# Kernel optimization log

Measured on AMD Instinct MI355X. Metric: run time of the kernel, lower is better.

Reference implementation:

```python
import jax, jax.numpy as jnp
import numpy as np

N_NODES = 50000
N_EDGES = 800000
F_DIM = 35   # num_features = in_channels = out_channels
K_HOPS = 3   # num_filters (diffusion order)


def _dconv(xcat, src, dst, w_fwd, w_bwd, theta, bias, n):
    """Dual-direction diffusion convolution: sum_k T_fwd^k X theta[0,k] + T_bwd^k X theta[1,k] + b.
    xcat: [n, Cin]; theta: [2, K, Cin, Cout]; w_fwd/w_bwd: [E] normalized edge weights."""
    out = xcat @ (theta[0, 0] + theta[1, 0]) + bias  # k=0 term (identity hop)
    xf = xcat
    xb = xcat
    for k in range(1, theta.shape[1]):
        # forward diffusion: aggregate src -> dst with out-degree normalization
        xf = jax.ops.segment_sum(w_fwd[:, None] * xf[src], dst, num_segments=n)
        # backward diffusion: aggregate dst -> src with in-degree normalization
        xb = jax.ops.segment_sum(w_bwd[:, None] * xb[dst], src, num_segments=n)
        out = out + xf @ theta[0, k] + xb @ theta[1, k]
    return out


def _cell(x, h, src, dst, wf, wb, tz, bz, tr, br, tc, bc, n):
    """DCRNN GRU cell with diffusion convolutions as the gate transforms."""
    xh = jnp.concatenate([x, h], axis=-1)  # [n, 2F]
    z = jax.nn.sigmoid(_dconv(xh, src, dst, wf, wb, tz, bz, n))
    r = jax.nn.sigmoid(_dconv(xh, src, dst, wf, wb, tr, br, n))
    c = jnp.tanh(_dconv(jnp.concatenate([x, r * h], axis=-1), src, dst, wf, wb, tc, bc, n))
    return z * h + (1.0 - z) * c


def setup_inputs() -> dict:
    key = jax.random.key(0)
    ks = jax.random.split(key, 12)
    x = jax.random.normal(ks[0], (N_NODES, F_DIM), dtype=jnp.float32)
    edge_index = jax.random.randint(ks[1], (2, N_EDGES), 0, N_NODES)
    edge_weight = jax.random.uniform(ks[2], (N_EDGES,), dtype=jnp.float32)
    cin = 2 * F_DIM
    s = 1.0 / np.sqrt(cin)
    u = lambda k, sh: jax.random.uniform(k, sh, jnp.float32, -s, s)
    theta_z = u(ks[3], (2, K_HOPS, cin, F_DIM)); b_z = u(ks[4], (F_DIM,))
    theta_r = u(ks[5], (2, K_HOPS, cin, F_DIM)); b_r = u(ks[6], (F_DIM,))
    theta_c = u(ks[7], (2, K_HOPS, cin, F_DIM)); b_c = u(ks[8], (F_DIM,))
    sl = 1.0 / np.sqrt(F_DIM)
    W_lin = jax.random.uniform(ks[9], (F_DIM, 1), jnp.float32, -sl, sl)
    b_lin = jax.random.uniform(ks[10], (1,), jnp.float32, -sl, sl)
    return dict(x=x, edge_index=edge_index, edge_weight=edge_weight,
                theta_z=theta_z, b_z=b_z, theta_r=theta_r, b_r=b_r,
                theta_c=theta_c, b_c=b_c, W_lin=W_lin, b_lin=b_lin)


def reference(x, edge_index, edge_weight, theta_z, b_z, theta_r, b_r, theta_c, b_c, W_lin, b_lin):
    n = x.shape[0]
    src, dst = edge_index[0], edge_index[1]
    # learned/normalized adjacency A (forward + backward transition weights)
    deg_out = jax.ops.segment_sum(edge_weight, src, num_segments=n)
    deg_in = jax.ops.segment_sum(edge_weight, dst, num_segments=n)
    wf = edge_weight / jnp.where(deg_out[src] > 0, deg_out[src], 1.0)
    wb = edge_weight / jnp.where(deg_in[dst] > 0, deg_in[dst], 1.0)
    A = jnp.stack([wf, wb])  # [2, E]
    h = jnp.zeros_like(x)
    # recurrent cell called twice (second call reuses hidden state and A)
    h = _cell(x, h, src, dst, wf, wb, theta_z, b_z, theta_r, b_r, theta_c, b_c, n)
    h = _cell(x, h, src, dst, wf, wb, theta_z, b_z, theta_r, b_r, theta_c, b_c, n)
    out = jax.nn.relu(h @ W_lin + b_lin)  # [n, 1]
    return out, A
```

## Files before the change

### kernel.cpp

```cpp
#include <hip/hip_runtime.h>
#include <hip/hip_fp16.h>

#define NF 35
#define HS 36
#define TMAT 2450
#define ZCOLS 384
#define ZUSED 360
#define CCOLS 192
#define CUSED 180


__global__ void degree2_k(const int* __restrict__ src, const int* __restrict__ dst,
                          unsigned int* __restrict__ cntF2, unsigned int* __restrict__ cntB2,
                          int* __restrict__ rankF, int* __restrict__ rankB, int E) {
    int e = blockIdx.x * blockDim.x + threadIdx.x;
    if (e < E) {
        int d = dst[e], s = src[e];
        int shd = (d & 1) * 16, shs = (s & 1) * 16;
        unsigned int o1 = atomicAdd(&cntF2[d >> 1], 1u << shd);
        rankF[e] = (int)((o1 >> shd) & 0xFFFFu);
        unsigned int o2 = atomicAdd(&cntB2[s >> 1], 1u << shs);
        rankB[e] = (int)((o2 >> shs) & 0xFFFFu);
    }
}

__global__ __launch_bounds__(1024) void scan2_k(const unsigned int* __restrict__ cntF2,
                                                const unsigned int* __restrict__ cntB2,
                                                int* __restrict__ rowF,
                                                int* __restrict__ rowB, int n) {
    const unsigned int* cnt = blockIdx.x ? cntB2 : cntF2;
    int* row = blockIdx.x ? rowB : rowF;
    __shared__ int wsum[16];
    __shared__ int carry_s;
    int lane = threadIdx.x & 63, wid = threadIdx.x >> 6;
    if (threadIdx.x == 0) carry_s = 0;
    __syncthreads();
    for (int base = 0; base < n; base += 1024) {
        int i = base + threadIdx.x;
        int v = 0;
        if (i < n) v = (int)((cnt[i >> 1] >> ((i & 1) * 16)) & 0xFFFFu);
        int s = v;
        for (int off = 1; off < 64; off <<= 1) {
            int t = __shfl_up(s, off, 64);
            if (lane >= off) s += t;
        }
        if (lane == 63) wsum[wid] = s;
        __syncthreads();
        if (wid == 0) {
            int t = (lane < 16) ? wsum[lane] : 0;
            int ss = t;
            for (int off = 1; off < 16; off <<= 1) {
                int u = __shfl_up(ss, off, 64);
                if (lane >= off) ss += u;
            }
            if (lane < 16) wsum[lane] = ss - t;
        }
        __syncthreads();
        if (i < n) row[i] = carry_s + wsum[wid] + s - v;
        __syncthreads();
        if (threadIdx.x == 1023) carry_s += wsum[15] + s;
        __syncthreads();
    }
    if (threadIdx.x == 0) row[n] = carry_s;
}

__global__ void scatter2_k(const int* __restrict__ src, const int* __restrict__ dst,
                           const float* __restrict__ w,
                           const int* __restrict__ rankF, const int* __restrict__ rankB,
                           const int* __restrict__ rowF, const int* __restrict__ rowB,
                           int2* __restrict__ pairF, int2* __restrict__ pairB, int E) {
    int e = blockIdx.x * blockDim.x + threadIdx.x;
    if (e < E) {
        int s = src[e], d = dst[e];
        int wb = __float_as_int(w[e]);
        pairF[rowF[d] + rankF[e]] = make_int2(s, wb);
        pairB[rowB[s] + rankB[e]] = make_int2(d, wb);
    }
}

__global__ void segdeg_k(const int* __restrict__ rowF, const int* __restrict__ rowB,
                         const int2* __restrict__ pairF, const int2* __restrict__ pairB,
                         float* __restrict__ deg_in, float* __restrict__ deg_out, int n) {
    int i = blockIdx.x * blockDim.x + threadIdx.x;
    if (i >= n) return;
    float a = 0.f;
    for (int p = rowF[i]; p < rowF[i + 1]; ++p) a += __int_as_float(pairF[p].y);
    deg_in[i] = a;
    float b = 0.f;
    for (int p = rowB[i]; p < rowB[i + 1]; ++p) b += __int_as_float(pairB[p].y);
    deg_out[i] = b;
}

__global__ void norm_k(const int* __restrict__ src, const int* __restrict__ dst,
                       const float* __restrict__ w, const float* __restrict__ deg_out,
                       const float* __restrict__ deg_in,
                       const int2* __restrict__ pairF, const int2* __restrict__ pairB,
                       unsigned int* __restrict__ pFp, unsigned int* __restrict__ pBp,
                       float* __restrict__ wf, float* __restrict__ wb, int E) {
    int e = blockIdx.x * blockDim.x + threadIdx.x;
    if (e >= E) return;
    float ww = w[e];
    float a = deg_out[src[e]];
    float b = deg_in[dst[e]];
    wf[e] = ww / (a > 0.f ? a : 1.f);
    wb[e] = ww / (b > 0.f ? b : 1.f);
    int2 pa = pairF[e];
    float da = deg_out[pa.x];
    float wa = __int_as_float(pa.y) / (da > 0.f ? da : 1.f);
    pFp[e] = (unsigned int)pa.x |
             ((unsigned int)__half_as_ushort(__float2half_rn(wa)) << 16);
    int2 pb = pairB[e];
    float db = deg_in[pb.x];
    float wbv = __int_as_float(pb.y) / (db > 0.f ? db : 1.f);
    pBp[e] = (unsigned int)pb.x |
             ((unsigned int)__half_as_ushort(__float2half_rn(wbv)) << 16);
}


__global__ void pack_k(const float* __restrict__ tz, const float* __restrict__ tr_,
                       const float* __restrict__ tc, const float* __restrict__ bz,
                       const float* __restrict__ br, const float* __restrict__ bc,
                       float* __restrict__ PZ, float* __restrict__ PC) {
    int i = blockIdx.x * 256 + threadIdx.x;
    const int tot1 = 71 * ZCOLS;
    if (i < tot1) {
        int r = i / ZCOLS, j = i - r * ZCOLS;
        int s = j / 36, jl = j - s * 36;
        float v = 0.f;
        if (s < 10 && jl < 35) {
            int zr = s & 1;
            const float* th = zr ? tr_ : tz;
            int grp = s >> 1;
            if (r < 70) {
                if (grp == 0) v = th[r * 35 + jl] + th[3 * TMAT + r * 35 + jl];
                else {
                    int off = (grp == 1) ? 1 : (grp == 2) ? 2 : (grp == 3) ? 4 : 5;
                    v = th[off * TMAT + r * 35 + jl];
                }
            } else if (grp == 0) {
                v = zr ? br[jl] : bz[jl];
            }
        }
        PZ[i] = v;
    } else {
        int i2 = i - tot1;
        if (i2 < 71 * CCOLS) {
            int r = i2 / CCOLS, j = i2 - r * CCOLS;
            int s = j / 36, jl = j - s * 36;
            float v = 0.f;
            if (s < 5 && jl < 35) {
                if (r < 70) {
                    if (s == 0) v = tc[r * 35 + jl] + tc[3 * TMAT + r * 35 + jl];
                    else {
                        int off = (s == 1) ? 1 : (s == 2) ? 2 : (s == 3) ? 4 : 5;
                        v = tc[off * TMAT + r * 35 + jl];
                    }
                } else if (s == 0) v = bc[jl];
            }
            PC[i2] = v;
        }
    }
}


__device__ __forceinline__ uint2 pack4h(float4 a) {
    __half2 lo = __floats2half2_rn(a.x, a.y);
    __half2 hi = __floats2half2_rn(a.z, a.w);
    uint2 r;
    r.x = *(unsigned int*)&lo;
    r.y = *(unsigned int*)&hi;
    return r;
}

__device__ __forceinline__ void fma2h(float* a, unsigned int v, float w) {
    float2 f = __half22float2(*(__half2*)&v);
    a[0] += w * f.x;
    a[1] += w * f.y;
}

__device__ __forceinline__ void fma4u2(float* a, uint2 v, float w) {
    fma2h(a, v.x, w);
    fma2h(a + 2, v.y, w);
}

__device__ __forceinline__ void ld4h(float* a, const char* p) {
    uint2 v = *(const uint2*)p;
    a[0] = 0.f; a[1] = 0.f; a[2] = 0.f; a[3] = 0.f;
    fma4u2(a, v, 1.f);
}

__device__ __forceinline__ void st4h(const float* a, char* p) {
    *(uint2*)p = pack4h(make_float4(a[0], a[1], a[2], a[3]));
}

__device__ __forceinline__ float hw(unsigned int e) {
    return __half2float(__ushort_as_half((unsigned short)(e >> 16)));
}

__device__ __forceinline__ void gath8(float* acc, const char* slab, int off,
                                      const int* __restrict__ rp,
                                      const unsigned int* __restrict__ pp, int row) {
    int p = rp[row], p1 = rp[row + 1];
    for (; p + 3 < p1; p += 4) {
        unsigned int e0 = pp[p], e1 = pp[p + 1], e2 = pp[p + 2], e3 = pp[p + 3];
        uint2 v0 = *(const uint2*)(slab + (size_t)(e0 & 0xFFFFu) * 72 + off);
        uint2 v1 = *(const uint2*)(slab + (size_t)(e1 & 0xFFFFu) * 72 + off);
        uint2 v2 = *(const uint2*)(slab + (size_t)(e2 & 0xFFFFu) * 72 + off);
        uint2 v3 = *(const uint2*)(slab + (size_t)(e3 & 0xFFFFu) * 72 + off);
        fma4u2(acc, v0, hw(e0));
        fma4u2(acc, v1, hw(e1));
        fma4u2(acc, v2, hw(e2));
        fma4u2(acc, v3, hw(e3));
    }
    for (; p < p1; ++p) {
        unsigned int e0 = pp[p];
        uint2 v0 = *(const uint2*)(slab + (size_t)(e0 & 0xFFFFu) * 72 + off);
        fma4u2(acc, v0, hw(e0));
    }
}


template <int WCOLS, int USED>
__device__ __forceinline__ void gemm_store(const float* sxr, const float* __restrict__ W,
                                           char* OUT, size_t slb, int grow, bool valid,
                                           int wid, int kdim) {
#pragma unroll
    for (int jt = 0; jt < WCOLS / 64; ++jt) {
        int j0 = __builtin_amdgcn_readfirstlane(jt * 64 + wid * 16);
        if (j0 >= USED) continue;
        const float4* bw = (const float4*)(W + (size_t)70 * WCOLS + j0);
        float4 a0 = bw[0], a1 = bw[1], a2 = bw[2], a3 = bw[3];
        for (int c = 0; c < kdim; ++c) {
            float v = sxr[c];
            const float4* wr = (const float4*)(W + (size_t)c * WCOLS + j0);
            float4 w0 = wr[0], w1 = wr[1], w2 = wr[2], w3 = wr[3];
            a0.x += v * w0.x; a0.y += v * w0.y; a0.z += v * w0.z; a0.w += v * w0.w;
            a1.x += v * w1.x; a1.y += v * w1.y; a1.z += v * w1.z; a1.w += v * w1.w;
            a2.x += v * w2.x; a2.y += v * w2.y; a2.z += v * w2.z; a2.w += v * w2.w;
            a3.x += v * w3.x; a3.y += v * w3.y; a3.z += v * w3.z; a3.w += v * w3.w;
        }
        if (valid) {
            float4 as[4] = {a0, a1, a2, a3};
#pragma unroll
            for (int g = 0; g < 4; ++g) {
                int jc = j0 + 4 * g;
                if (jc >= USED) break;
                int s = jc / 36, off = jc - s * 36;
                *(uint2*)(OUT + (size_t)s * slb + (size_t)grow * 72 + off * 2) =
                    pack4h(as[g]);
            }
        }
    }
}


template <int H0>
__global__ __launch_bounds__(256) void mm_z_k(const float* __restrict__ x,
                                              const float* __restrict__ h,
                                              const float* __restrict__ W,
                                              char* __restrict__ zS, int n) {
    __shared__ float sx[64 * 73];
    int row0 = blockIdx.x * 64;
    for (int t = threadIdx.x; t < 64 * 35; t += 256) {
        int rl = t / 35, c = t - rl * 35;
        int grow = row0 + rl;
        sx[rl * 73 + c] = (grow < n) ? x[(size_t)grow * 35 + c] : 0.f;
    }
    if (!H0) {
        for (int t = threadIdx.x; t < 64 * 35; t += 256) {
            int rl = t / 35, c = t - rl * 35;
            int grow = row0 + rl;
            sx[rl * 73 + 35 + c] = (grow < n) ? h[(size_t)grow * HS + c] : 0.f;
        }
    }
    __syncthreads();
    int lane = threadIdx.x & 63;
    int wid = threadIdx.x >> 6;
    int grow = row0 + lane;
    gemm_store<ZCOLS, ZUSED>(&sx[lane * 73], W, zS, (size_t)n * 72, grow, grow < n,
                             wid, H0 ? 35 : 70);
}


__global__ __launch_bounds__(256) void mmc_k(const float* __restrict__ x,
                                             const float* __restrict__ h,
                                             const char* __restrict__ zS,
                                             const float* __restrict__ W,
                                             char* __restrict__ cS, int n) {
    __shared__ float sx[64 * 73];
    size_t slb = (size_t)n * 72;
    int row0 = blockIdx.x * 64;
    for (int t = threadIdx.x; t < 64 * 35; t += 256) {
        int rl = t / 35, c = t - rl * 35;
        int grow = row0 + rl;
        sx[rl * 73 + c] = (grow < n) ? x[(size_t)grow * 35 + c] : 0.f;
    }
    for (int t = threadIdx.x; t < 64 * 35; t += 256) {
        int rl = t / 35, c = t - rl * 35;
        int grow = row0 + rl;
        float v = 0.f;
        if (grow < n) {
            float r = __half2float(*(const __half*)(zS + slb + (size_t)grow * 72 + 2 * c));
            v = r * h[(size_t)grow * HS + c];
        }
        sx[rl * 73 + 35 + c] = v;
    }
    __syncthreads();
    int lane = threadIdx.x & 63;
    int wid = threadIdx.x >> 6;
    int grow = row0 + lane;
    gemm_store<CCOLS, CUSED>(&sx[lane * 73], W, cS, slb, grow, grow < n, wid, 70);
}


__global__ __launch_bounds__(256) void hopAz_k(char* __restrict__ zS,
                                               const int* __restrict__ rowF,
                                               const int* __restrict__ rowB,
                                               const unsigned int* __restrict__ pF,
                                               const unsigned int* __restrict__ pB,
                                               int n) {
    int i = blockIdx.x * 256 + threadIdx.x;
    if (i >= n * 9) return;
    size_t slb = (size_t)n * 72;
    int pass = blockIdx.y;
    const int* rp = (pass < 2) ? rowF : rowB;
    const unsigned int* pp = (pass < 2) ? pF : pB;
    int dstS = (pass == 0) ? 2 : (pass == 1) ? 3 : (pass == 2) ? 6 : 7;
    int srcS = dstS + 2;
    int row = i / 9, t = i - row * 9;
    int off = 8 * t;
    char* wp = zS + (size_t)dstS * slb + (size_t)row * 72 + off;
    float acc[4];
    ld4h(acc, wp);
    gath8(acc, zS + (size_t)srcS * slb, off, rp, pp, row);
    st4h(acc, wp);
}

__global__ __launch_bounds__(256) void hopBz_k(char* __restrict__ zS,
                                               const int* __restrict__ rowF,
                                               const int* __restrict__ rowB,
                                               const unsigned int* __restrict__ pF,
                                               const unsigned int* __restrict__ pB,
                                               int n) {
    int i = blockIdx.x * 256 + threadIdx.x;
    if (i >= n * 9) return;
    size_t slb = (size_t)n * 72;
    int g = blockIdx.y;
    int row = i / 9, t = i - row * 9;
    int off = 8 * t;
    char* wp = zS + (size_t)g * slb + (size_t)row * 72 + off;
    float acc[4];
    ld4h(acc, wp);
    gath8(acc, zS + (size_t)(2 + g) * slb, off, rowF, pF, row);
    gath8(acc, zS + (size_t)(6 + g) * slb, off, rowB, pB, row);
#pragma unroll
    for (int k = 0; k < 4; ++k) acc[k] = 1.f / (1.f + expf(-acc[k]));
    st4h(acc, wp);
}

__global__ __launch_bounds__(256) void hopAc_k(char* __restrict__ cS,
                                               const int* __restrict__ rowF,
                                               const int* __restrict__ rowB,
                                               const unsigned int* __restrict__ pF,
                                               const unsigned int* __restrict__ pB,
                                               int n) {
    int i = blockIdx.x * 256 + threadIdx.x;
    if (i >= n * 9) return;
    size_t slb = (size_t)n * 72;
    int pass = blockIdx.y;
    const int* rp = pass ? rowB : rowF;
    const unsigned int* pp = pass ? pB : pF;
    int dstS = pass ? 3 : 1;
    int srcS = pass ? 4 : 2;
    int row = i / 9, t = i - row * 9;
    int off = 8 * t;
    char* wp = cS + (size_t)dstS * slb + (size_t)row * 72 + off;
    float acc[4];
    ld4h(acc, wp);
    gath8(acc, cS + (size_t)srcS * slb, off, rp, pp, row);
    st4h(acc, wp);
}

__global__ __launch_bounds__(256) void hopBcg_k(const char* __restrict__ cS,
                                                const char* __restrict__ zS,
                                                const int* __restrict__ rowF,
                                                const int* __restrict__ rowB,
                                                const unsigned int* __restrict__ pF,
                                                const unsigned int* __restrict__ pB,
                                                float* __restrict__ h, int n) {
    int i = blockIdx.x * 256 + threadIdx.x;
    if (i >= n * 9) return;
    size_t slb = (size_t)n * 72;
    int row = i / 9, t = i - row * 9;
    int off = 8 * t;
    float acc[4];
    ld4h(acc, cS + (size_t)row * 72 + off);
    gath8(acc, cS + slb, off, rowF, pF, row);
    gath8(acc, cS + 3 * slb, off, rowB, pB, row);
    float zv[4];
    ld4h(zv, zS + (size_t)row * 72 + off);
    float* hp = h + (size_t)row * HS + 4 * t;
    float4 h4 = *(float4*)hp;
    float hv[4] = {h4.x, h4.y, h4.z, h4.w};
#pragma unroll
    for (int k = 0; k < 4; ++k) {
        float c = tanhf(acc[k]);
        hv[k] = zv[k] * hv[k] + (1.f - zv[k]) * c;
    }
    *(float4*)hp = make_float4(hv[0], hv[1], hv[2], hv[3]);
}


__global__ void final_k(const float* __restrict__ h, const float* __restrict__ Wl,
                        const float* __restrict__ bl, float* __restrict__ out, int n) {
    int i = blockIdx.x * blockDim.x + threadIdx.x;
    if (i < n) {
        float s = bl[0];
        const float* hr = h + (size_t)i * HS;
#pragma unroll
        for (int j = 0; j < NF; j++) s += hr[j] * Wl[j];
        out[i] = fmaxf(s, 0.f);
    }
}


extern "C" void kernel_launch(void* const* d_in, const int* in_sizes, int n_in,
                              void* d_out, int out_size, void* d_ws, size_t ws_size,
                              hipStream_t stream) {
    const float* x   = (const float*)d_in[0];
    const int*   ei  = (const int*)d_in[1];
    const float* w   = (const float*)d_in[2];
    const float* tz  = (const float*)d_in[3];
    const float* bz  = (const float*)d_in[4];
    const float* tr_ = (const float*)d_in[5];
    const float* br  = (const float*)d_in[6];
    const float* tc  = (const float*)d_in[7];
    const float* bc  = (const float*)d_in[8];
    const float* Wl  = (const float*)d_in[9];
    const float* bl  = (const float*)d_in[10];

    const int n = in_sizes[0] / NF;
    const int E = in_sizes[2];
    const int* src = ei;
    const int* dst = ei + E;

    float* out = (float*)d_out;
    float* wf = out + n;
    float* wb = wf + E;

    char* p = (char*)d_ws;
    auto alloc = [&](size_t bytes) {
        char* r = p;
        p += (bytes + 15) & ~(size_t)15;
        return r;
    };
    int2* pairF = (int2*)alloc((size_t)E * 8);
    int2* pairB = (int2*)alloc((size_t)E * 8);
    unsigned int* pFp = (unsigned int*)alloc((size_t)E * 4);
    unsigned int* pBp = (unsigned int*)alloc((size_t)E * 4);
    int* rowF = (int*)alloc((size_t)(n + 1) * 4);
    int* rowB = (int*)alloc((size_t)(n + 1) * 4);
    unsigned int* cntF2 = (unsigned int*)alloc((size_t)((n + 1) / 2 + 4) * 4);
    unsigned int* cntB2 = (unsigned int*)alloc((size_t)((n + 1) / 2 + 4) * 4);
    float* deg_in  = (float*)alloc((size_t)n * 4);
    float* deg_out = (float*)alloc((size_t)n * 4);
    float* h  = (float*)alloc((size_t)n * HS * 4);
    char* zS  = alloc((size_t)n * 72 * 10);
    char* cS  = alloc((size_t)n * 72 * 5);
    float* PZ = (float*)alloc((size_t)71 * ZCOLS * 4);
    float* PC = (float*)alloc((size_t)71 * CCOLS * 4);
    int* rankF = (int*)zS;
    int* rankB = rankF + E;

    const int gridE = (E + 255) / 256;
    const int gridN = (n + 255) / 256;
    const int g64 = (n + 63) / 64;
    const int g9 = (n * 9 + 255) / 256;
    const size_t cntBytes = ((size_t)((n + 1) / 2 + 4) * 4 + 15) & ~(size_t)15;

    hipMemsetAsync(cntF2, 0, 2 * cntBytes, stream);
    hipMemsetAsync(h, 0, (size_t)n * HS * sizeof(float), stream);
    degree2_k<<<gridE, 256, 0, stream>>>(src, dst, cntF2, cntB2, rankF, rankB, E);
    scan2_k<<<2, 1024, 0, stream>>>(cntF2, cntB2, rowF, rowB, n);
    scatter2_k<<<gridE, 256, 0, stream>>>(src, dst, w, rankF, rankB, rowF, rowB,
                                          pairF, pairB, E);
    segdeg_k<<<gridN, 256, 0, stream>>>(rowF, rowB, pairF, pairB, deg_in, deg_out, n);
    norm_k<<<gridE, 256, 0, stream>>>(src, dst, w, deg_out, deg_in, pairF, pairB,
                                      pFp, pBp, wf, wb, E);
    pack_k<<<(71 * (ZCOLS + CCOLS) + 255) / 256, 256, 0, stream>>>(tz, tr_, tc,
                                                                   bz, br, bc, PZ, PC);

    mm_z_k<1><<<g64, 256, 0, stream>>>(x, h, PZ, zS, n);
    hopAz_k<<<dim3(g9, 4), 256, 0, stream>>>(zS, rowF, rowB, pFp, pBp, n);
    hopBz_k<<<dim3(g9, 2), 256, 0, stream>>>(zS, rowF, rowB, pFp, pBp, n);
    mmc_k<<<g64, 256, 0, stream>>>(x, h, zS, PC, cS, n);
    hopAc_k<<<dim3(g9, 2), 256, 0, stream>>>(cS, rowF, rowB, pFp, pBp, n);
    hopBcg_k<<<g9, 256, 0, stream>>>(cS, zS, rowF, rowB, pFp, pBp, h, n);
    mm_z_k<0><<<g64, 256, 0, stream>>>(x, h, PZ, zS, n);
    hopAz_k<<<dim3(g9, 4), 256, 0, stream>>>(zS, rowF, rowB, pFp, pBp, n);
    hopBz_k<<<dim3(g9, 2), 256, 0, stream>>>(zS, rowF, rowB, pFp, pBp, n);
    mmc_k<<<g64, 256, 0, stream>>>(x, h, zS, PC, cS, n);
    hopAc_k<<<dim3(g9, 2), 256, 0, stream>>>(cS, rowF, rowB, pFp, pBp, n);
    hopBcg_k<<<g9, 256, 0, stream>>>(cS, zS, rowF, rowB, pFp, pBp, h, n);

    final_k<<<gridN, 256, 0, stream>>>(h, Wl, bl, out, n);
}
```

Baseline: 676.2 us.

## Split GEMM column tiles across grid and pair z/r gathers per edge

The GEMM kernels now assign one 64-column tile per block via a second grid dimension instead of looping over all column tiles in each block, raising parallelism. The z and r hop gathers are merged so each edge index and weight is read once and used for two slabs, halving index traffic. The c-gate hop A kernel now does both directions in one thread instead of two grid passes. Each sx tile is now reloaded into shared memory once per column block, and the per-thread gather loads grow.

```diff
diff --git a/kernel.cpp b/kernel.cpp
--- a/kernel.cpp
+++ b/kernel.cpp
@@ -219,36 +219,61 @@
     }
 }
 
+__device__ __forceinline__ void gath8x2(float* a1, float* a2, const char* s1b,
+                                        const char* s2b, int off,
+                                        const int* __restrict__ rp,
+                                        const unsigned int* __restrict__ pp, int row) {
+    int p = rp[row], p1 = rp[row + 1];
+    for (; p + 3 < p1; p += 4) {
+        unsigned int e0 = pp[p], e1 = pp[p + 1], e2 = pp[p + 2], e3 = pp[p + 3];
+        size_t b0 = (size_t)(e0 & 0xFFFFu) * 72 + off;
+        size_t b1 = (size_t)(e1 & 0xFFFFu) * 72 + off;
+        size_t b2 = (size_t)(e2 & 0xFFFFu) * 72 + off;
+        size_t b3 = (size_t)(e3 & 0xFFFFu) * 72 + off;
+        uint2 x0 = *(const uint2*)(s1b + b0), y0 = *(const uint2*)(s2b + b0);
+        uint2 x1 = *(const uint2*)(s1b + b1), y1 = *(const uint2*)(s2b + b1);
+        uint2 x2 = *(const uint2*)(s1b + b2), y2 = *(const uint2*)(s2b + b2);
+        uint2 x3 = *(const uint2*)(s1b + b3), y3 = *(const uint2*)(s2b + b3);
+        float w0 = hw(e0), w1 = hw(e1), w2 = hw(e2), w3 = hw(e3);
+        fma4u2(a1, x0, w0); fma4u2(a2, y0, w0);
+        fma4u2(a1, x1, w1); fma4u2(a2, y1, w1);
+        fma4u2(a1, x2, w2); fma4u2(a2, y2, w2);
+        fma4u2(a1, x3, w3); fma4u2(a2, y3, w3);
+    }
+    for (; p < p1; ++p) {
+        unsigned int e0 = pp[p];
+        size_t b0 = (size_t)(e0 & 0xFFFFu) * 72 + off;
+        float w0 = hw(e0);
+        fma4u2(a1, *(const uint2*)(s1b + b0), w0);
+        fma4u2(a2, *(const uint2*)(s2b + b0), w0);
+    }
+}
+
 
 template <int WCOLS, int USED>
-__device__ __forceinline__ void gemm_store(const float* sxr, const float* __restrict__ W,
-                                           char* OUT, size_t slb, int grow, bool valid,
-                                           int wid, int kdim) {
+__device__ __forceinline__ void gemm_tile(const float* sxr, const float* __restrict__ W,
+                                          char* OUT, size_t slb, int grow, bool valid,
+                                          int j0, int kdim) {
+    if (j0 >= USED) return;
+    const float4* bw = (const float4*)(W + (size_t)70 * WCOLS + j0);
+    float4 a0 = bw[0], a1 = bw[1], a2 = bw[2], a3 = bw[3];
+    for (int c = 0; c < kdim; ++c) {
+        float v = sxr[c];
+        const float4* wr = (const float4*)(W + (size_t)c * WCOLS + j0);
+        float4 w0 = wr[0], w1 = wr[1], w2 = wr[2], w3 = wr[3];
+        a0.x += v * w0.x; a0.y += v * w0.y; a0.z += v * w0.z; a0.w += v * w0.w;
+        a1.x += v * w1.x; a1.y += v * w1.y; a1.z += v * w1.z; a1.w += v * w1.w;
+        a2.x += v * w2.x; a2.y += v * w2.y; a2.z += v * w2.z; a2.w += v * w2.w;
+        a3.x += v * w3.x; a3.y += v * w3.y; a3.z += v * w3.z; a3.w += v * w3.w;
+    }
+    if (valid) {
+        float4 as[4] = {a0, a1, a2, a3};
 #pragma unroll
-    for (int jt = 0; jt < WCOLS / 64; ++jt) {
-        int j0 = __builtin_amdgcn_readfirstlane(jt * 64 + wid * 16);
-        if (j0 >= USED) continue;
-        const float4* bw = (const float4*)(W + (size_t)70 * WCOLS + j0);
-        float4 a0 = bw[0], a1 = bw[1], a2 = bw[2], a3 = bw[3];
-        for (int c = 0; c < kdim; ++c) {
-            float v = sxr[c];
-            const float4* wr = (const float4*)(W + (size_t)c * WCOLS + j0);
-            float4 w0 = wr[0], w1 = wr[1], w2 = wr[2], w3 = wr[3];
-            a0.x += v * w0.x; a0.y += v * w0.y; a0.z += v * w0.z; a0.w += v * w0.w;
-            a1.x += v * w1.x; a1.y += v * w1.y; a1.z += v * w1.z; a1.w += v * w1.w;
-            a2.x += v * w2.x; a2.y += v * w2.y; a2.z += v * w2.z; a2.w += v * w2.w;
-            a3.x += v * w3.x; a3.y += v * w3.y; a3.z += v * w3.z; a3.w += v * w3.w;
-        }
-        if (valid) {
-            float4 as[4] = {a0, a1, a2, a3};
-#pragma unroll
-            for (int g = 0; g < 4; ++g) {
-                int jc = j0 + 4 * g;
-                if (jc >= USED) break;
-                int s = jc / 36, off = jc - s * 36;
-                *(uint2*)(OUT + (size_t)s * slb + (size_t)grow * 72 + off * 2) =
-                    pack4h(as[g]);
-            }
+        for (int g = 0; g < 4; ++g) {
+            int jc = j0 + 4 * g;
+            if (jc >= USED) break;
+            int s = jc / 36, off = jc - s * 36;
+            *(uint2*)(OUT + (size_t)s * slb + (size_t)grow * 72 + off * 2) = pack4h(as[g]);
         }
     }
 }
@@ -277,8 +302,9 @@
     int lane = threadIdx.x & 63;
     int wid = threadIdx.x >> 6;
     int grow = row0 + lane;
-    gemm_store<ZCOLS, ZUSED>(&sx[lane * 73], W, zS, (size_t)n * 72, grow, grow < n,
-                             wid, H0 ? 35 : 70);
+    int j0 = __builtin_amdgcn_readfirstlane(blockIdx.y * 64 + wid * 16);
+    gemm_tile<ZCOLS, ZUSED>(&sx[lane * 73], W, zS, (size_t)n * 72, grow, grow < n,
+                            j0, H0 ? 35 : 70);
 }
 
 
@@ -309,53 +335,62 @@
     int lane = threadIdx.x & 63;
     int wid = threadIdx.x >> 6;
     int grow = row0 + lane;
-    gemm_store<CCOLS, CUSED>(&sx[lane * 73], W, cS, slb, grow, grow < n, wid, 70);
-}
-
-
-__global__ __launch_bounds__(256) void hopAz_k(char* __restrict__ zS,
-                                               const int* __restrict__ rowF,
-                                               const int* __restrict__ rowB,
-                                               const unsigned int* __restrict__ pF,
-                                               const unsigned int* __restrict__ pB,
-                                               int n) {
+    int j0 = __builtin_amdgcn_readfirstlane(blockIdx.y * 64 + wid * 16);
+    gemm_tile<CCOLS, CUSED>(&sx[lane * 73], W, cS, slb, grow, grow < n, j0, 70);
+}
+
+
+__global__ __launch_bounds__(256) void hopAzr_k(char* __restrict__ zS,
+                                                const int* __restrict__ rowF,
+                                                const int* __restrict__ rowB,
+                                                const unsigned int* __restrict__ pF,
+                                                const unsigned int* __restrict__ pB,
+                                                int n) {
     int i = blockIdx.x * 256 + threadIdx.x;
     if (i >= n * 9) return;
     size_t slb = (size_t)n * 72;
     int pass = blockIdx.y;
-    const int* rp = (pass < 2) ? rowF : rowB;
-    const unsigned int* pp = (pass < 2) ? pF : pB;
-    int dstS = (pass == 0) ? 2 : (pass == 1) ? 3 : (pass == 2) ? 6 : 7;
-    int srcS = dstS + 2;
+    const int* rp = pass ? rowB : rowF;
+    const unsigned int* pp = pass ? pB : pF;
+    int dz = pass ? 6 : 2;
     int row = i / 9, t = i - row * 9;
     int off = 8 * t;
-    char* wp = zS + (size_t)dstS * slb + (size_t)row * 72 + off;
-    float acc[4];
-    ld4h(acc, wp);
-    gath8(acc, zS + (size_t)srcS * slb, off, rp, pp, row);
-    st4h(acc, wp);
-}
-
-__global__ __launch_bounds__(256) void hopBz_k(char* __restrict__ zS,
-                                               const int* __restrict__ rowF,
-                                               const int* __restrict__ rowB,
-                                               const unsigned int* __restrict__ pF,
-                                               const unsigned int* __restrict__ pB,
-                                               int n) {
+    char* wpz = zS + (size_t)dz * slb + (size_t)row * 72 + off;
+    char* wpr = wpz + slb;
+    float az[4], ar[4];
+    ld4h(az, wpz);
+    ld4h(ar, wpr);
+    gath8x2(az, ar, zS + (size_t)(dz + 2) * slb, zS + (size_t)(dz + 3) * slb,
+            off, rp, pp, row);
+    st4h(az, wpz);
+    st4h(ar, wpr);
+}
+
+__global__ __launch_bounds__(256) void hopBzr_k(char* __restrict__ zS,
+                                                const int* __restrict__ rowF,
+                                                const int* __restrict__ rowB,
+                                                const unsigned int* __restrict__ pF,
+                                                const unsigned int* __restrict__ pB,
+                                                int n) {
     int i = blockIdx.x * 256 + threadIdx.x;
     if (i >= n * 9) return;
     size_t slb = (size_t)n * 72;
-    int g = blockIdx.y;
     int row = i / 9, t = i - row * 9;
     int off = 8 * t;
-    char* wp = zS + (size_t)g * slb + (size_t)row * 72 + off;
-    float acc[4];
-    ld4h(acc, wp);
-    gath8(acc, zS + (size_t)(2 + g) * slb, off, rowF, pF, row);
-    gath8(acc, zS + (size_t)(6 + g) * slb, off, rowB, pB, row);
+    char* wpz = zS + (size_t)row * 72 + off;
+    char* wpr = wpz + slb;
+    float az[4], ar[4];
+    ld4h(az, wpz);
+    ld4h(ar, wpr);
+    gath8x2(az, ar, zS + 2 * slb, zS + 3 * slb, off, rowF, pF, row);
+    gath8x2(az, ar, zS + 6 * slb, zS + 7 * slb, off, rowB, pB, row);
 #pragma unroll
-    for (int k = 0; k < 4; ++k) acc[k] = 1.f / (1.f + expf(-acc[k]));
-    st4h(acc, wp);
+    for (int k = 0; k < 4; ++k) {
+        az[k] = 1.f / (1.f + expf(-az[k]));
+        ar[k] = 1.f / (1.f + expf(-ar[k]));
+    }
+    st4h(az, wpz);
+    st4h(ar, wpr);
 }
 
 __global__ __launch_bounds__(256) void hopAc_k(char* __restrict__ cS,
@@ -367,18 +402,22 @@
     int i = blockIdx.x * 256 + threadIdx.x;
     if (i >= n * 9) return;
     size_t slb = (size_t)n * 72;
-    int pass = blockIdx.y;
-    const int* rp = pass ? rowB : rowF;
-    const unsigned int* pp = pass ? pB : pF;
-    int dstS = pass ? 3 : 1;
-    int srcS = pass ? 4 : 2;
     int row = i / 9, t = i - row * 9;
     int off = 8 * t;
-    char* wp = cS + (size_t)dstS * slb + (size_t)row * 72 + off;
-    float acc[4];
-    ld4h(acc, wp);
-    gath8(acc, cS + (size_t)srcS * slb, off, rp, pp, row);
-    st4h(acc, wp);
+    {
+        char* wp = cS + slb + (size_t)row * 72 + off;
+        float acc[4];
+        ld4h(acc, wp);
+        gath8(acc, cS + 2 * slb, off, rowF, pF, row);
+        st4h(acc, wp);
+    }
+    {
+        char* wp = cS + 3 * slb + (size_t)row * 72 + off;
+        float acc[4];
+        ld4h(acc, wp);
+        gath8(acc, cS + 4 * slb, off, rowB, pB, row);
+        st4h(acc, wp);
+    }
 }
 
 __global__ __launch_bounds__(256) void hopBcg_k(const char* __restrict__ cS,
@@ -490,18 +529,17 @@
     pack_k<<<(71 * (ZCOLS + CCOLS) + 255) / 256, 256, 0, stream>>>(tz, tr_, tc,
                                                                    bz, br, bc, PZ, PC);
 
-    mm_z_k<1><<<g64, 256, 0, stream>>>(x, h, PZ, zS, n);
-    hopAz_k<<<dim3(g9, 4), 256, 0, stream>>>(zS, rowF, rowB, pFp, pBp, n);
-    hopBz_k<<<dim3(g9, 2), 256, 0, stream>>>(zS, rowF, rowB, pFp, pBp, n);
-    mmc_k<<<g64, 256, 0, stream>>>(x, h, zS, PC, cS, n);
-    hopAc_k<<<dim3(g9, 2), 256, 0, stream>>>(cS, rowF, rowB, pFp, pBp, n);
-    hopBcg_k<<<g9, 256, 0, stream>>>(cS, zS, rowF, rowB, pFp, pBp, h, n);
-    mm_z_k<0><<<g64, 256, 0, stream>>>(x, h, PZ, zS, n);
-    hopAz_k<<<dim3(g9, 4), 256, 0, stream>>>(zS, rowF, rowB, pFp, pBp, n);
-    hopBz_k<<<dim3(g9, 2), 256, 0, stream>>>(zS, rowF, rowB, pFp, pBp, n);
-    mmc_k<<<g64, 256, 0, stream>>>(x, h, zS, PC, cS, n);
-    hopAc_k<<<dim3(g9, 2), 256, 0, stream>>>(cS, rowF, rowB, pFp, pBp, n);
-    hopBcg_k<<<g9, 256, 0, stream>>>(cS, zS, rowF, rowB, pFp, pBp, h, n);
+    for (int cellit = 0; cellit < 2; ++cellit) {
+        if (cellit == 0)
+            mm_z_k<1><<<dim3(g64, 6), 256, 0, stream>>>(x, h, PZ, zS, n);
+        else
+            mm_z_k<0><<<dim3(g64, 6), 256, 0, stream>>>(x, h, PZ, zS, n);
+        hopAzr_k<<<dim3(g9, 2), 256, 0, stream>>>(zS, rowF, rowB, pFp, pBp, n);
+        hopBzr_k<<<g9, 256, 0, stream>>>(zS, rowF, rowB, pFp, pBp, n);
+        mmc_k<<<dim3(g64, 3), 256, 0, stream>>>(x, h, zS, PC, cS, n);
+        hopAc_k<<<g9, 256, 0, stream>>>(cS, rowF, rowB, pFp, pBp, n);
+        hopBcg_k<<<g9, 256, 0, stream>>>(cS, zS, rowF, rowB, pFp, pBp, h, n);
+    }
 
     final_k<<<gridN, 256, 0, stream>>>(h, Wl, bl, out, n);
 }
```

Measured after the change: 724.1 us. 1.07x slower.
